# Performance work log

Hardware: AMD Instinct MI355X
Metric: run time of the kernel (lower is better)

Reference implementation:

```python
import jax, jax.numpy as jnp
import numpy as np

MERGE_K = 3   # merge_kernel
DS_K = 3      # ds_kernel (avg-pool kernel)
STRIDE = 2


def _unfold(x, kernel, stride):
    """Torch-style F.pad + unfold(2).unfold(3): x [N,C,H,W] -> [N,Ho,Wo,K,C],
    K = kernel**2 in row-major (dh, dw) order, padding = kernel//2 with zeros."""
    pad = kernel // 2
    N, C, H, W = x.shape
    Ho, Wo = H // stride, W // stride
    xp = jnp.pad(x, ((0, 0), (0, 0), (pad, pad), (pad, pad)))
    pats = [
        xp[:, :, di:di + stride * (Ho - 1) + 1:stride,
               dj:dj + stride * (Wo - 1) + 1:stride]
        for di in range(kernel) for dj in range(kernel)
    ]
    p = jnp.stack(pats, axis=-1)          # [N,C,Ho,Wo,K]
    return p.transpose(0, 2, 3, 4, 1)     # [N,Ho,Wo,K,C]


def setup_inputs() -> dict:
    key = jax.random.key(0)
    x = jax.random.normal(key, (32, 768, 56, 56), dtype=jnp.float32)
    return {"x": x}


def reference(x):
    # compute_kq=False: k = q = x
    # AvgPool2d(3, stride=2, padding=1), count_include_pad=True -> mean over
    # zero-padded 3x3 windows == mean over K axis of the unfold.
    q = _unfold(x, DS_K, STRIDE).mean(axis=3)   # [N,Ho,Wo,C]
    kv = _unfold(x, MERGE_K, STRIDE)            # [N,Ho,Wo,K,C]; k and v are identical unfolds of x
    scores = jnp.einsum('nhwc,nhwkc->nhwk', q, kv) / MERGE_K  # divide by merge_kernel (=3), per source
    attn = jax.nn.softmax(scores, axis=-1)      # [N,Ho,Wo,K]
    y = jnp.einsum('nhwk,nhwkc->nhwc', attn, kv)  # weighted merge
    return y.transpose(0, 3, 1, 2)              # [N,C,Ho,Wo]
```

## Files before the change

### kernel.cpp

```cpp
#include <hip/hip_runtime.h>


constexpr int N_  = 32;
constexpr int C_  = 768;
constexpr int H_  = 56;
constexpr int W_  = 56;
constexpr int HO_ = 28;
constexpr int WO_ = 28;
constexpr int NPIX = N_ * HO_ * WO_;

constexpr int K1_CHUNKS = 4;
constexpr int K1_CCH    = C_ / K1_CHUNKS;
constexpr int K1_SC     = 16;
constexpr int K1_NSUB   = K1_CCH / K1_SC;
constexpr int K1_TW     = 58;
constexpr int K1_TR     = 5;

__global__ __launch_bounds__(256)
void scores_kernel(const float* __restrict__ x, float* __restrict__ scores) {
    __shared__ float tile[K1_SC * K1_TR * K1_TW];
    __shared__ float sred[4 * 56 * 9];

    const int tid   = threadIdx.x;
    const int blk   = blockIdx.x;
    const int chunk = blk / (N_ * 14);
    const int rem   = blk - chunk * (N_ * 14);
    const int n     = rem / 14;
    const int ho2   = rem - n * 14;
    const int c0    = chunk * K1_CCH;
    const int row0  = 4 * ho2 - 1;

    for (int i = tid; i < K1_SC * K1_TR * K1_TW; i += 256) tile[i] = 0.f;

    const int g  = tid >> 6;
    const int p  = tid & 63;
    const int hr = p >> 5;
    const int wo = p & 31;
    const bool act = wo < WO_;

    float acc[9];
#pragma unroll
    for (int k = 0; k < 9; ++k) acc[k] = 0.f;

    const float* xb = x + ((size_t)n * C_ + c0) * (H_ * W_);

    for (int sub = 0; sub < K1_NSUB; ++sub) {
        __syncthreads();
        for (int i = tid; i < K1_SC * K1_TR * 14; i += 256) {
            int c    = i / (K1_TR * 14);
            int r2   = i - c * (K1_TR * 14);
            int r    = r2 / 14;
            int kk   = r2 - r * 14;
            int grow = row0 + r;
            if (grow >= 0) {
                float4 v = *(const float4*)(xb + ((size_t)(sub * K1_SC + c) * H_ + grow) * W_ + 4 * kk);
                float* d = &tile[(c * K1_TR + r) * K1_TW + 1 + 4 * kk];
                d[0] = v.x; d[1] = v.y; d[2] = v.z; d[3] = v.w;
            }
        }
        __syncthreads();
        if (act) {
#pragma unroll
            for (int cc = 0; cc < K1_SC / 4; ++cc) {
                const int c = cc * 4 + g;
                const float* tp = &tile[(c * K1_TR + 2 * hr) * K1_TW + 2 * wo];
                float2 r0 = *(const float2*)(tp);
                float  w2 = tp[2];
                float2 r1 = *(const float2*)(tp + K1_TW);
                float  w5 = tp[K1_TW + 2];
                float2 r2 = *(const float2*)(tp + 2 * K1_TW);
                float  w8 = tp[2 * K1_TW + 2];
                float w0 = r0.x, w1 = r0.y, w3 = r1.x, w4 = r1.y, w6 = r2.x, w7 = r2.y;
                float q = ((w0 + w1) + (w2 + w3)) + ((w4 + w5) + (w6 + w7)) + w8;
                acc[0] += q * w0; acc[1] += q * w1; acc[2] += q * w2;
                acc[3] += q * w3; acc[4] += q * w4; acc[5] += q * w5;
                acc[6] += q * w6; acc[7] += q * w7; acc[8] += q * w8;
            }
        }
    }

    if (act) {
        const int s = hr * 28 + wo;
#pragma unroll
        for (int k = 0; k < 9; ++k) sred[(g * 56 + s) * 9 + k] = acc[k];
    }
    __syncthreads();
    for (int i = tid; i < 56 * 9; i += 256) {
        int s = i / 9, k = i - s * 9;
        float t = sred[s * 9 + k]         + sred[(56 + s) * 9 + k]
                + sred[(112 + s) * 9 + k] + sred[(168 + s) * 9 + k];
        int hrr = s / 28, woo = s - hrr * 28;
        int ho  = 2 * ho2 + hrr;
        atomicAdd(&scores[(((size_t)n * HO_ + ho) * WO_ + woo) * 9 + k], t * (1.f / 27.f));
    }
}

__global__ __launch_bounds__(256)
void softmax_kernel(float* __restrict__ scores) {
    __shared__ float sbuf[256 * 9];
    const int tid = threadIdx.x;
    float4* gb = (float4*)(scores + (size_t)blockIdx.x * (256 * 9));
    float4* lb = (float4*)sbuf;
    for (int i = tid; i < 576; i += 256) lb[i] = gb[i];
    __syncthreads();
    float v[9];
    float* s = sbuf + tid * 9;
#pragma unroll
    for (int k = 0; k < 9; ++k) v[k] = s[k];
    float m = v[0];
#pragma unroll
    for (int k = 1; k < 9; ++k) m = fmaxf(m, v[k]);
    float d = 0.f;
#pragma unroll
    for (int k = 0; k < 9; ++k) { v[k] = __expf(v[k] - m); d += v[k]; }
    float inv = 1.f / d;
#pragma unroll
    for (int k = 0; k < 9; ++k) s[k] = v[k] * inv;
    __syncthreads();
    for (int i = tid; i < 576; i += 256) gb[i] = lb[i];
}

constexpr int K3_TW = 58;

__global__ __launch_bounds__(256)
void merge_kernel(const float* __restrict__ x, const float* __restrict__ attn,
                  float* __restrict__ out) {
    __shared__ float tile_raw[4 + K3_TW * K3_TW];
    __shared__ float attn_s[HO_ * WO_ * 9];
    float* tile = tile_raw + 4;

    const int tid = threadIdx.x;
    const int blk = blockIdx.x;
    const int n   = blk / C_;
    const int c   = blk - n * C_;

    for (int i = tid; i < 4 + K3_TW * K3_TW; i += 256) tile_raw[i] = 0.f;
    __syncthreads();

    const float* xp = x + ((size_t)n * C_ + c) * (H_ * W_);
    for (int i = tid; i < 784; i += 256) {
        int r  = i / 14;
        int kk = i - r * 14;
        float4 v = *(const float4*)(xp + (size_t)r * W_ + 4 * kk);
        float* d = &tile[(r + 1) * K3_TW + 4 * kk];
        d[0] = v.x; d[1] = v.y; d[2] = v.z; d[3] = v.w;
    }
    const float4* ag = (const float4*)(attn + (size_t)n * (HO_ * WO_ * 9));
    float4* as = (float4*)attn_s;
    for (int i = tid; i < (HO_ * WO_ * 9) / 4; i += 256) as[i] = ag[i];
    __syncthreads();

    float* op = out + ((size_t)n * C_ + c) * (HO_ * WO_);
    for (int p = tid; p < HO_ * WO_; p += 256) {
        int ho = p / WO_, wo = p - ho * WO_;
        const float* a  = &attn_s[p * 9];
        const float* tp = &tile[(size_t)(2 * ho) * K3_TW + 2 * wo - 1];
        float y = a[0] * tp[0]           + a[1] * tp[1]             + a[2] * tp[2]
                + a[3] * tp[K3_TW]       + a[4] * tp[K3_TW + 1]     + a[5] * tp[K3_TW + 2]
                + a[6] * tp[2 * K3_TW]   + a[7] * tp[2 * K3_TW + 1] + a[8] * tp[2 * K3_TW + 2];
        op[p] = y;
    }
}

extern "C" void kernel_launch(void* const* d_in, const int* in_sizes, int n_in,
                              void* d_out, int out_size, void* d_ws, size_t ws_size,
                              hipStream_t stream) {
    const float* x   = (const float*)d_in[0];
    float* out       = (float*)d_out;
    float* scores    = (float*)d_ws;

    hipMemsetAsync(d_ws, 0, (size_t)NPIX * 9 * sizeof(float), stream);
    scores_kernel<<<dim3(K1_CHUNKS * N_ * 14), dim3(256), 0, stream>>>(x, scores);
    softmax_kernel<<<dim3(NPIX / 256), dim3(256), 0, stream>>>(scores);
    merge_kernel<<<dim3(N_ * C_), dim3(256), 0, stream>>>(x, scores, out);
}
```

Measured before the change: 624.3 us.

## Split merge kernel into half-image blocks and realign scores tile

```diff
diff --git a/kernel.cpp b/kernel.cpp
--- a/kernel.cpp
+++ b/kernel.cpp
@@ -18,8 +18,9 @@
 
 __global__ __launch_bounds__(256)
 void scores_kernel(const float* __restrict__ x, float* __restrict__ scores) {
-    __shared__ float tile[K1_SC * K1_TR * K1_TW];
+    __shared__ float tile_raw[4 + K1_SC * K1_TR * K1_TW];
     __shared__ float sred[4 * 56 * 9];
+    float* tile = tile_raw + 4;
 
     const int tid   = threadIdx.x;
     const int blk   = blockIdx.x;
@@ -30,7 +31,7 @@
     const int c0    = chunk * K1_CCH;
     const int row0  = 4 * ho2 - 1;
 
-    for (int i = tid; i < K1_SC * K1_TR * K1_TW; i += 256) tile[i] = 0.f;
+    for (int i = tid; i < 4 + K1_SC * K1_TR * K1_TW; i += 256) tile_raw[i] = 0.f;
 
     const int g  = tid >> 6;
     const int p  = tid & 63;
@@ -54,7 +55,7 @@
             int grow = row0 + r;
             if (grow >= 0) {
                 float4 v = *(const float4*)(xb + ((size_t)(sub * K1_SC + c) * H_ + grow) * W_ + 4 * kk);
-                float* d = &tile[(c * K1_TR + r) * K1_TW + 1 + 4 * kk];
+                float* d = &tile[(c * K1_TR + r) * K1_TW + 4 * kk];
                 d[0] = v.x; d[1] = v.y; d[2] = v.z; d[3] = v.w;
             }
         }
@@ -63,14 +64,10 @@
 #pragma unroll
             for (int cc = 0; cc < K1_SC / 4; ++cc) {
                 const int c = cc * 4 + g;
-                const float* tp = &tile[(c * K1_TR + 2 * hr) * K1_TW + 2 * wo];
-                float2 r0 = *(const float2*)(tp);
-                float  w2 = tp[2];
-                float2 r1 = *(const float2*)(tp + K1_TW);
-                float  w5 = tp[K1_TW + 2];
-                float2 r2 = *(const float2*)(tp + 2 * K1_TW);
-                float  w8 = tp[2 * K1_TW + 2];
-                float w0 = r0.x, w1 = r0.y, w3 = r1.x, w4 = r1.y, w6 = r2.x, w7 = r2.y;
+                const float* tp = &tile[(c * K1_TR + 2 * hr) * K1_TW + 2 * wo - 1];
+                float w0 = tp[0],          w1 = tp[1],             w2 = tp[2];
+                float w3 = tp[K1_TW],      w4 = tp[K1_TW + 1],     w5 = tp[K1_TW + 2];
+                float w6 = tp[2 * K1_TW],  w7 = tp[2 * K1_TW + 1], w8 = tp[2 * K1_TW + 2];
                 float q = ((w0 + w1) + (w2 + w3)) + ((w4 + w5) + (w6 + w7)) + w8;
                 acc[0] += q * w0; acc[1] += q * w1; acc[2] += q * w2;
                 acc[3] += q * w3; acc[4] += q * w4; acc[5] += q * w5;
@@ -120,41 +117,48 @@
     for (int i = tid; i < 576; i += 256) gb[i] = lb[i];
 }
 
-constexpr int K3_TW = 58;
+constexpr int K3_ROWS = 29;
+constexpr int K3_TW   = 58;
 
 __global__ __launch_bounds__(256)
 void merge_kernel(const float* __restrict__ x, const float* __restrict__ attn,
                   float* __restrict__ out) {
-    __shared__ float tile_raw[4 + K3_TW * K3_TW];
-    __shared__ float attn_s[HO_ * WO_ * 9];
+    __shared__ float tile_raw[4 + K3_ROWS * K3_TW];
+    __shared__ float attn_s[14 * WO_ * 9];
     float* tile = tile_raw + 4;
 
     const int tid = threadIdx.x;
     const int blk = blockIdx.x;
-    const int n   = blk / C_;
-    const int c   = blk - n * C_;
+    const int n   = blk / (C_ * 2);
+    const int rem = blk - n * (C_ * 2);
+    const int c   = rem >> 1;
+    const int h   = rem & 1;
+    const int r0  = 28 * h - 1;
 
-    for (int i = tid; i < 4 + K3_TW * K3_TW; i += 256) tile_raw[i] = 0.f;
+    for (int i = tid; i < 4 + K3_ROWS * K3_TW; i += 256) tile_raw[i] = 0.f;
     __syncthreads();
 
     const float* xp = x + ((size_t)n * C_ + c) * (H_ * W_);
-    for (int i = tid; i < 784; i += 256) {
-        int r  = i / 14;
-        int kk = i - r * 14;
-        float4 v = *(const float4*)(xp + (size_t)r * W_ + 4 * kk);
-        float* d = &tile[(r + 1) * K3_TW + 4 * kk];
-        d[0] = v.x; d[1] = v.y; d[2] = v.z; d[3] = v.w;
+    for (int i = tid; i < K3_ROWS * 14; i += 256) {
+        int tr = i / 14;
+        int kk = i - tr * 14;
+        int grow = r0 + tr;
+        if (grow >= 0) {
+            float4 v = *(const float4*)(xp + (size_t)grow * W_ + 4 * kk);
+            float* d = &tile[tr * K3_TW + 4 * kk];
+            d[0] = v.x; d[1] = v.y; d[2] = v.z; d[3] = v.w;
+        }
     }
-    const float4* ag = (const float4*)(attn + (size_t)n * (HO_ * WO_ * 9));
+    const float4* ag = (const float4*)(attn + ((size_t)n * 784 + h * 392) * 9);
     float4* as = (float4*)attn_s;
-    for (int i = tid; i < (HO_ * WO_ * 9) / 4; i += 256) as[i] = ag[i];
+    for (int i = tid; i < 882; i += 256) as[i] = ag[i];
     __syncthreads();
 
-    float* op = out + ((size_t)n * C_ + c) * (HO_ * WO_);
-    for (int p = tid; p < HO_ * WO_; p += 256) {
-        int ho = p / WO_, wo = p - ho * WO_;
+    float* op = out + ((size_t)n * C_ + c) * (HO_ * WO_) + h * 392;
+    for (int p = tid; p < 392; p += 256) {
+        int ho_l = p / WO_, wo = p - ho_l * WO_;
         const float* a  = &attn_s[p * 9];
-        const float* tp = &tile[(size_t)(2 * ho) * K3_TW + 2 * wo - 1];
+        const float* tp = &tile[(size_t)(2 * ho_l) * K3_TW + 2 * wo - 1];
         float y = a[0] * tp[0]           + a[1] * tp[1]             + a[2] * tp[2]
                 + a[3] * tp[K3_TW]       + a[4] * tp[K3_TW + 1]     + a[5] * tp[K3_TW + 2]
                 + a[6] * tp[2 * K3_TW]   + a[7] * tp[2 * K3_TW + 1] + a[8] * tp[2 * K3_TW + 2];
@@ -172,5 +176,5 @@
     hipMemsetAsync(d_ws, 0, (size_t)NPIX * 9 * sizeof(float), stream);
     scores_kernel<<<dim3(K1_CHUNKS * N_ * 14), dim3(256), 0, stream>>>(x, scores);
     softmax_kernel<<<dim3(NPIX / 256), dim3(256), 0, stream>>>(scores);
-    merge_kernel<<<dim3(N_ * C_), dim3(256), 0, stream>>>(x, scores, out);
+    merge_kernel<<<dim3(N_ * C_ * 2), dim3(256), 0, stream>>>(x, scores, out);
 }
```

New measurement: 576.5 us. -7.7%, faster.
